# Kernel optimization log

Hardware: AMD Instinct MI355X
Metric: run time of the kernel (lower is better)

## Reference

```python
import jax, jax.numpy as jnp
import numpy as np

N_NODES = 50000
N_EDGES = 800000
N_GRAPHS = 64
IN_CH = 128
HID_CH = 128
OUT_CH = 2


def setup_inputs() -> dict:
    key = jax.random.key(0)
    k = jax.random.split(key, 7)
    x = jax.random.normal(k[0], (N_NODES, IN_CH), dtype=jnp.float32)
    edge_index = jax.random.randint(k[1], (2, N_EDGES), 0, N_NODES, dtype=jnp.int64)
    batch = jnp.sort(jax.random.randint(k[2], (N_NODES,), 0, N_GRAPHS, dtype=jnp.int64))
    W1 = jax.random.normal(k[3], (IN_CH, HID_CH), dtype=jnp.float32) * 0.05
    b1 = jnp.zeros((HID_CH,), dtype=jnp.float32)
    W2 = jax.random.normal(k[4], (HID_CH, OUT_CH), dtype=jnp.float32) * 0.05
    b2 = jnp.zeros((OUT_CH,), dtype=jnp.float32)
    return {"x": x, "edge_index": edge_index, "batch": batch,
            "W1": W1, "b1": b1, "W2": W2, "b2": b2}


def gcn_conv(x, edge_index, W, b):
    """PyG GCNConv: add self-loops, symmetric D^{-1/2}(A+I)D^{-1/2} aggregation of XW, plus bias."""
    n = x.shape[0]
    loop = jnp.arange(n, dtype=edge_index.dtype)
    src = jnp.concatenate([edge_index[0], loop])  # [E+N]
    dst = jnp.concatenate([edge_index[1], loop])
    ones = jnp.ones_like(dst, dtype=x.dtype)
    deg = jax.ops.segment_sum(ones, dst, num_segments=n)      # in-degree incl. self-loop (>=1)
    d_inv_sqrt = jax.lax.rsqrt(deg)
    norm = d_inv_sqrt[src] * d_inv_sqrt[dst]                  # [E+N]
    h = x @ W                                                 # [N, out]
    msg = h[src] * norm[:, None]                              # gather + scale
    out = jax.ops.segment_sum(msg, dst, num_segments=n)       # scatter-add
    return out + b


def global_mean_pool(x, batch, num_graphs):
    sums = jax.ops.segment_sum(x, batch, num_segments=num_graphs)
    cnt = jax.ops.segment_sum(jnp.ones((x.shape[0],), dtype=x.dtype), batch, num_segments=num_graphs)
    return sums / jnp.maximum(cnt, 1.0)[:, None]


def reference(x, edge_index, batch, W1, b1, W2, b2):
    h = jax.nn.relu(gcn_conv(x, edge_index, W1, b1))
    h = gcn_conv(h, edge_index, W2, b2)
    out = global_mean_pool(h, batch, N_GRAPHS)  # [G, out_channels]
    # dropout in eval mode == identity
    return out
```

## Files before the change

kernel.cpp:

```cpp
#include <hip/hip_runtime.h>


#define NGRAPH 64
#define CH 128
#define BSUB 384
#define NCOPY 8
#define BCAPT (BSUB * NCOPY)

typedef float f32x4 __attribute__((ext_vector_type(4)));
typedef _Float16 f16x8 __attribute__((ext_vector_type(8)));
typedef _Float16 f16x4 __attribute__((ext_vector_type(4)));
typedef _Float16 f16x2 __attribute__((ext_vector_type(2)));

__global__ void k_init(int* __restrict__ bcur8, int* __restrict__ row_start,
                       float* __restrict__ gsum, int* __restrict__ gcnt,
                       int NB, int N, int E) {
    int i = blockIdx.x * blockDim.x + threadIdx.x;
    if (i < NB * NCOPY) bcur8[i] = 0;
    if (i == 0) row_start[N] = E;
    if (i < 2 * NGRAPH) gsum[i] = 0.f;
    if (i < NGRAPH) gcnt[i] = 0;
}

__global__ __launch_bounds__(256) void k_bin(const int* __restrict__ src,
                                             const int* __restrict__ dst,
                                             int* __restrict__ bcur8,
                                             unsigned int* __restrict__ tmp,
                                             int E, int EPB) {
    __shared__ int hist[512];
    __shared__ int gbase[512];
    __shared__ int cur[512];
    int t = threadIdx.x;
    int e0 = blockIdx.x * EPB;
    int e1 = min(E, e0 + EPB);
    for (int i = t; i < 512; i += 256) { hist[i] = 0; cur[i] = 0; }
    __syncthreads();
    for (int e = e0 + t; e < e1; e += 256)
        atomicAdd(&hist[dst[e] >> 7], 1);
    __syncthreads();
    int copy = blockIdx.x & (NCOPY - 1);
    for (int b = t; b < 512; b += 256) {
        int hc = hist[b];
        if (hc) gbase[b] = atomicAdd(&bcur8[b * NCOPY + copy], hc);
    }
    __syncthreads();
    for (int e = e0 + t; e < e1; e += 256) {
        int d = dst[e];
        int b = d >> 7;
        int li = atomicAdd(&cur[b], 1);
        int pos = gbase[b] + li;
        if (pos < BSUB)
            tmp[(size_t)b * BCAPT + copy * BSUB + pos] =
                ((unsigned)(d & 127) << 25) | (unsigned)src[e];
    }
}

__global__ __launch_bounds__(256) void k_hist(const unsigned int* __restrict__ tmp,
                                              const int* __restrict__ bcur8,
                                              int* __restrict__ deg,
                                              float* __restrict__ dinv, int N) {
    __shared__ int hist[128];
    int b = blockIdx.x, t = threadIdx.x;
    if (t < 128) hist[t] = 0;
    __syncthreads();
    const unsigned int* tb = tmp + (size_t)b * BCAPT;
    for (int c = 0; c < NCOPY; c++) {
        int cnt = min(bcur8[b * NCOPY + c], BSUB);
        const unsigned int* tp = tb + c * BSUB;
        for (int e = t; e < cnt; e += 256) atomicAdd(&hist[tp[e] >> 25], 1);
    }
    __syncthreads();
    int n = b * 128 + t;
    if (t < 128 && n < N) {
        int d = hist[t] + 1;
        deg[n] = d;
        dinv[n] = rsqrtf((float)d);
    }
}

__global__ void k_scan_a(const int* __restrict__ deg, int* __restrict__ row_start,
                         int* __restrict__ bsum, int N) {
    __shared__ int tmp[256];
    int t = threadIdx.x;
    int i = blockIdx.x * 256 + t;
    int v = (i < N) ? (deg[i] - 1) : 0;
    int val = v;
    tmp[t] = val;
    __syncthreads();
    for (int off = 1; off < 256; off <<= 1) {
        int add = (t >= off) ? tmp[t - off] : 0;
        __syncthreads();
        val += add;
        tmp[t] = val;
        __syncthreads();
    }
    if (i < N) row_start[i] = val - v;
    if (t == 255) bsum[blockIdx.x] = val;
}

__global__ void k_scan_b(const int* __restrict__ bsum, int* __restrict__ boff, int nb) {
    __shared__ int tmp[256];
    int t = threadIdx.x;
    int v = (t < nb) ? bsum[t] : 0;
    int val = v;
    tmp[t] = val;
    __syncthreads();
    for (int off = 1; off < 256; off <<= 1) {
        int add = (t >= off) ? tmp[t - off] : 0;
        __syncthreads();
        val += add;
        tmp[t] = val;
        __syncthreads();
    }
    if (t < nb) boff[t] = val - v;
}

__global__ void k_scan_c(int* __restrict__ row_start, const int* __restrict__ boff, int N) {
    int i = blockIdx.x * blockDim.x + threadIdx.x;
    if (i < N) row_start[i] += boff[blockIdx.x];
}

__global__ __launch_bounds__(256) void k_place(const unsigned int* __restrict__ tmp,
                                               const int* __restrict__ bcur8,
                                               const int* __restrict__ row_start,
                                               int* __restrict__ csr, int N) {
    __shared__ int lcur[128];
    int b = blockIdx.x, t = threadIdx.x;
    int nb0 = b * 128;
    int base = row_start[nb0];
    if (t < 128) {
        int n = nb0 + t;
        lcur[t] = ((n < N) ? row_start[n] : 0) - base;
    }
    __syncthreads();
    const unsigned int* tb = tmp + (size_t)b * BCAPT;
    for (int c = 0; c < NCOPY; c++) {
        int cnt = min(bcur8[b * NCOPY + c], BSUB);
        const unsigned int* tp = tb + c * BSUB;
        for (int e = t; e < cnt; e += 256) {
            unsigned p = tp[e];
            int pos = atomicAdd(&lcur[p >> 25], 1);
            csr[base + pos] = (int)(p & 0x01FFFFFFu);
        }
    }
}

__global__ __launch_bounds__(256) void k_gemm1(const float* __restrict__ X,
                                               const float* __restrict__ W1,
                                               const float* __restrict__ dinv,
                                               _Float16* __restrict__ H, int N) {
    __shared__ _Float16 Xs[64 * 136];
    __shared__ _Float16 Ws[128 * 136];
    int t = threadIdx.x;
    int row0 = blockIdx.x * 64;
    const float4* Xv = (const float4*)X;
    const float4* Wv = (const float4*)W1;

    #pragma unroll
    for (int i = 0; i < 8; i++) {
        int gi = t + i * 256;
        int r = gi >> 5, c4 = gi & 31;
        int gr = row0 + r;
        float4 v = (gr < N) ? Xv[(size_t)gr * 32 + c4] : make_float4(0.f, 0.f, 0.f, 0.f);
        f16x4 hv = {(_Float16)v.x, (_Float16)v.y, (_Float16)v.z, (_Float16)v.w};
        *(f16x4*)&Xs[r * 136 + 4 * c4] = hv;
    }
    #pragma unroll
    for (int i = 0; i < 4; i++) {
        int b = t + i * 256;
        int kb = b >> 5, cb = b & 31;
        float4 r0 = Wv[(4 * kb + 0) * 32 + cb];
        float4 r1 = Wv[(4 * kb + 1) * 32 + cb];
        float4 r2 = Wv[(4 * kb + 2) * 32 + cb];
        float4 r3 = Wv[(4 * kb + 3) * 32 + cb];
        f16x4 c0v = {(_Float16)r0.x, (_Float16)r1.x, (_Float16)r2.x, (_Float16)r3.x};
        f16x4 c1v = {(_Float16)r0.y, (_Float16)r1.y, (_Float16)r2.y, (_Float16)r3.y};
        f16x4 c2v = {(_Float16)r0.z, (_Float16)r1.z, (_Float16)r2.z, (_Float16)r3.z};
        f16x4 c3v = {(_Float16)r0.w, (_Float16)r1.w, (_Float16)r2.w, (_Float16)r3.w};
        *(f16x4*)&Ws[(4 * cb + 0) * 136 + 4 * kb] = c0v;
        *(f16x4*)&Ws[(4 * cb + 1) * 136 + 4 * kb] = c1v;
        *(f16x4*)&Ws[(4 * cb + 2) * 136 + 4 * kb] = c2v;
        *(f16x4*)&Ws[(4 * cb + 3) * 136 + 4 * kb] = c3v;
    }
    __syncthreads();

    int w = t >> 6, l = t & 63;
    int r0w = w * 16;
    int lr = l & 15, lk = (l >> 4) * 8;
    f32x4 acc[8] = {};
    #pragma unroll
    for (int k0 = 0; k0 < 128; k0 += 32) {
        f16x8 a = *(const f16x8*)&Xs[(r0w + lr) * 136 + k0 + lk];
        #pragma unroll
        for (int c = 0; c < 8; c++) {
            f16x8 bf = *(const f16x8*)&Ws[(c * 16 + lr) * 136 + k0 + lk];
            acc[c] = __builtin_amdgcn_mfma_f32_16x16x32_f16(a, bf, acc[c], 0, 0, 0);
        }
    }
    float dv[4];
    #pragma unroll
    for (int q = 0; q < 4; q++) {
        int gr = row0 + r0w + (l >> 4) * 4 + q;
        dv[q] = (gr < N) ? dinv[gr] : 0.f;
    }
    __syncthreads();
    #pragma unroll
    for (int c = 0; c < 8; c++)
        #pragma unroll
        for (int q = 0; q < 4; q++)
            Xs[(r0w + (l >> 4) * 4 + q) * 136 + c * 16 + lr] = (_Float16)(acc[c][q] * dv[q]);
    __syncthreads();
    f16x2* Hv = (f16x2*)H;
    #pragma unroll
    for (int i = 0; i < 16; i++) {
        int gi = t + i * 256;
        int r = gi >> 6, cp = gi & 63;
        int gr = row0 + r;
        if (gr < N) Hv[(size_t)gr * 64 + cp] = *(f16x2*)&Xs[r * 136 + 2 * cp];
    }
}

__global__ __launch_bounds__(256) void k_layer1(const _Float16* __restrict__ h,
                                                const int* __restrict__ csr,
                                                const int* __restrict__ row_start,
                                                const float* __restrict__ dinv,
                                                const float* __restrict__ b1,
                                                const float* __restrict__ W2,
                                                float* __restrict__ h2, int N) {
    int n = (blockIdx.x * 256 + threadIdx.x) >> 6;
    int l = threadIdx.x & 63;
    if (n >= N) return;
    const f16x2* hv = (const f16x2*)h;
    float dn = dinv[n];
    f16x2 self = hv[(size_t)n * 64 + l];
    float acc0 = (float)self.x, acc1 = (float)self.y;
    int base = row_start[n];
    int cnt = row_start[n + 1] - base;
    for (int c0 = 0; c0 < cnt; c0 += 64) {
        int m = cnt - c0; if (m > 64) m = 64;
        int idx = (c0 + l < cnt) ? csr[base + c0 + l] : 0;
        int j = 0;
        int jm = m & ~7;
        for (; j < jm; j += 8) {
            int s0 = __shfl(idx, j + 0), s1 = __shfl(idx, j + 1);
            int s2 = __shfl(idx, j + 2), s3 = __shfl(idx, j + 3);
            int s4 = __shfl(idx, j + 4), s5 = __shfl(idx, j + 5);
            int s6 = __shfl(idx, j + 6), s7 = __shfl(idx, j + 7);
            f16x2 v0 = hv[(size_t)s0 * 64 + l];
            f16x2 v1 = hv[(size_t)s1 * 64 + l];
            f16x2 v2 = hv[(size_t)s2 * 64 + l];
            f16x2 v3 = hv[(size_t)s3 * 64 + l];
            f16x2 v4 = hv[(size_t)s4 * 64 + l];
            f16x2 v5 = hv[(size_t)s5 * 64 + l];
            f16x2 v6 = hv[(size_t)s6 * 64 + l];
            f16x2 v7 = hv[(size_t)s7 * 64 + l];
            acc0 += (float)v0.x; acc1 += (float)v0.y;
            acc0 += (float)v1.x; acc1 += (float)v1.y;
            acc0 += (float)v2.x; acc1 += (float)v2.y;
            acc0 += (float)v3.x; acc1 += (float)v3.y;
            acc0 += (float)v4.x; acc1 += (float)v4.y;
            acc0 += (float)v5.x; acc1 += (float)v5.y;
            acc0 += (float)v6.x; acc1 += (float)v6.y;
            acc0 += (float)v7.x; acc1 += (float)v7.y;
        }
        for (; j < m; ++j) {
            int s = __shfl(idx, j);
            f16x2 v = hv[(size_t)s * 64 + l];
            acc0 += (float)v.x; acc1 += (float)v.y;
        }
    }
    float2 bb = ((const float2*)b1)[l];
    float v0 = fmaxf(fmaf(dn, acc0, bb.x), 0.f);
    float v1 = fmaxf(fmaf(dn, acc1, bb.y), 0.f);
    float4 w2 = ((const float4*)W2)[l];
    float p0 = fmaf(v0, w2.x, v1 * w2.z);
    float p1 = fmaf(v0, w2.y, v1 * w2.w);
    #pragma unroll
    for (int off = 32; off; off >>= 1) {
        p0 += __shfl_xor(p0, off);
        p1 += __shfl_xor(p1, off);
    }
    if (l == 0) ((float2*)h2)[n] = make_float2(p0 * dn, p1 * dn);
}

__global__ __launch_bounds__(256) void k_layer2_pool(const float* __restrict__ h2,
                                                     const int* __restrict__ csr,
                                                     const int* __restrict__ row_start,
                                                     const float* __restrict__ dinv,
                                                     const int* __restrict__ batch,
                                                     float* __restrict__ gsum,
                                                     int* __restrict__ gcnt, int N) {
    __shared__ float ssum[2 * NGRAPH];
    __shared__ int scnt[NGRAPH];
    int t = threadIdx.x;
    if (t < 2 * NGRAPH) ssum[t] = 0.f;
    if (t < NGRAPH) scnt[t] = 0;
    __syncthreads();
    int n = blockIdx.x * blockDim.x + t;
    if (n < N) {
        const float2* h2v = (const float2*)h2;
        float dn = dinv[n];
        float2 a = h2v[n];
        int base = row_start[n], end = row_start[n + 1];
        for (int e = base; e < end; e++) {
            float2 v = h2v[csr[e]];
            a.x += v.x;
            a.y += v.y;
        }
        a.x *= dn;
        a.y *= dn;
        int g = batch[n];
        atomicAdd(&ssum[g * 2 + 0], a.x);
        atomicAdd(&ssum[g * 2 + 1], a.y);
        atomicAdd(&scnt[g], 1);
    }
    __syncthreads();
    if (t < 2 * NGRAPH) atomicAdd(&gsum[t], ssum[t]);
    if (t < NGRAPH) atomicAdd(&gcnt[t], scnt[t]);
}

__global__ void k_final(const float* __restrict__ gsum, const int* __restrict__ gcnt,
                        const float* __restrict__ b2, float* __restrict__ out) {
    int t = threadIdx.x;
    if (t < 2 * NGRAPH) {
        int g = t >> 1, c = t & 1;
        float cnt = fmaxf((float)gcnt[g], 1.f);
        out[t] = gsum[t] / cnt + b2[c];
    }
}

extern "C" void kernel_launch(void* const* d_in, const int* in_sizes, int n_in,
                              void* d_out, int out_size, void* d_ws, size_t ws_size,
                              hipStream_t stream) {
    const float* x     = (const float*)d_in[0];
    const int*   ei    = (const int*)d_in[1];
    const int*   batch = (const int*)d_in[2];
    const float* W1    = (const float*)d_in[3];
    const float* b1    = (const float*)d_in[4];
    const float* W2    = (const float*)d_in[5];
    const float* b2    = (const float*)d_in[6];
    float* out = (float*)d_out;

    int N = in_sizes[0] / CH;
    int E = in_sizes[1] / 2;
    int NB = (N + 127) / 128;
    const int* esrc = ei;
    const int* edst = ei + E;

    char* w = (char*)d_ws;
    auto alloc = [&](size_t bytes) -> void* {
        void* p = (void*)w;
        w += (bytes + 255) & ~(size_t)255;
        return p;
    };
    _Float16* h      = (_Float16*)alloc((size_t)N * CH * sizeof(_Float16));
    int* deg         = (int*)  alloc((size_t)N * sizeof(int));
    float* dinv      = (float*)alloc((size_t)N * sizeof(float));
    int* row_start   = (int*)  alloc((size_t)(N + 1) * sizeof(int));
    int* csr         = (int*)  alloc((size_t)E * sizeof(int));
    float* h2        = (float*)alloc((size_t)N * 2 * sizeof(float));
    int* bcur8       = (int*)  alloc((size_t)NB * NCOPY * sizeof(int));
    int* bsum        = (int*)  alloc(256 * sizeof(int));
    int* boff        = (int*)  alloc(256 * sizeof(int));
    float* gsum      = (float*)alloc(128 * sizeof(float));
    int* gcnt        = (int*)  alloc(64 * sizeof(int));
    unsigned int* tmp = (unsigned int*)h;

    int nbN = (N + 255) / 256;
    int NCHUNK = 256;
    int EPB = (E + NCHUNK - 1) / NCHUNK;

    k_init  <<<nbN, 256, 0, stream>>>(bcur8, row_start, gsum, gcnt, NB, N, E);
    k_bin   <<<NCHUNK, 256, 0, stream>>>(esrc, edst, bcur8, tmp, E, EPB);
    k_hist  <<<NB,  256, 0, stream>>>(tmp, bcur8, deg, dinv, N);
    k_scan_a<<<nbN, 256, 0, stream>>>(deg, row_start, bsum, N);
    k_scan_b<<<1,   256, 0, stream>>>(bsum, boff, nbN);
    k_scan_c<<<nbN, 256, 0, stream>>>(row_start, boff, N);
    k_place <<<NB,  256, 0, stream>>>(tmp, bcur8, row_start, csr, N);
    k_gemm1 <<<(N + 63) / 64, 256, 0, stream>>>(x, W1, dinv, h, N);
    k_layer1<<<(N * 64 + 255) / 256, 256, 0, stream>>>(h, csr, row_start, dinv, b1, W2, h2, N);
    k_layer2_pool<<<nbN, 256, 0, stream>>>(h2, csr, row_start, dinv, batch, gsum, gcnt, N);
    k_final <<<1, 128, 0, stream>>>(gsum, gcnt, b2, out);
}
```

Baseline: 185.5 us.

## Fuse degree histogram, scan and CSR placement into one build kernel

Replaces the separate histogram, three-pass scan and placement kernels with a single-block bucket-total scan followed by one build kernel per bucket. That kernel computes degrees, a local scan, row starts, dinv and CSR placement together. W1 is also converted to transposed fp16 once in the init kernel, so each GEMM block copies it instead of reconverting it. This cuts kernel launches and global round-trips for deg and row_start, at the cost of a serial 512-thread scan kernel.

Result: faster. 174.9 us (-5.7%).

```diff
diff --git a/kernel.cpp b/kernel.cpp
--- a/kernel.cpp
+++ b/kernel.cpp
@@ -14,12 +14,17 @@
 
 __global__ void k_init(int* __restrict__ bcur8, int* __restrict__ row_start,
                        float* __restrict__ gsum, int* __restrict__ gcnt,
+                       const float* __restrict__ W1, _Float16* __restrict__ w1t,
                        int NB, int N, int E) {
     int i = blockIdx.x * blockDim.x + threadIdx.x;
     if (i < NB * NCOPY) bcur8[i] = 0;
     if (i == 0) row_start[N] = E;
     if (i < 2 * NGRAPH) gsum[i] = 0.f;
     if (i < NGRAPH) gcnt[i] = 0;
+    if (i < CH * CH) {
+        int k = i >> 7, c = i & 127;
+        w1t[c * CH + k] = (_Float16)W1[i];
+    }
 }
 
 __global__ __launch_bounds__(256) void k_bin(const int* __restrict__ src,
@@ -55,11 +60,35 @@
     }
 }
 
-__global__ __launch_bounds__(256) void k_hist(const unsigned int* __restrict__ tmp,
-                                              const int* __restrict__ bcur8,
-                                              int* __restrict__ deg,
-                                              float* __restrict__ dinv, int N) {
+__global__ __launch_bounds__(512) void k_bsum(const int* __restrict__ bcur8,
+                                              int* __restrict__ bbase, int NB) {
+    __shared__ int tmp[512];
+    int t = threadIdx.x;
+    int v = 0;
+    if (t < NB)
+        for (int c = 0; c < NCOPY; c++) v += min(bcur8[t * NCOPY + c], BSUB);
+    int val = v;
+    tmp[t] = val;
+    __syncthreads();
+    for (int off = 1; off < 512; off <<= 1) {
+        int add = (t >= off) ? tmp[t - off] : 0;
+        __syncthreads();
+        val += add;
+        tmp[t] = val;
+        __syncthreads();
+    }
+    if (t < NB) bbase[t] = val - v;
+}
+
+__global__ __launch_bounds__(256) void k_build(const unsigned int* __restrict__ tmp,
+                                               const int* __restrict__ bcur8,
+                                               const int* __restrict__ bbase,
+                                               int* __restrict__ row_start,
+                                               float* __restrict__ dinv,
+                                               int* __restrict__ csr, int N) {
     __shared__ int hist[128];
+    __shared__ int scan[128];
+    __shared__ int lcur[128];
     int b = blockIdx.x, t = threadIdx.x;
     if (t < 128) hist[t] = 0;
     __syncthreads();
@@ -70,70 +99,26 @@
         for (int e = t; e < cnt; e += 256) atomicAdd(&hist[tp[e] >> 25], 1);
     }
     __syncthreads();
-    int n = b * 128 + t;
-    if (t < 128 && n < N) {
-        int d = hist[t] + 1;
-        deg[n] = d;
-        dinv[n] = rsqrtf((float)d);
-    }
-}
-
-__global__ void k_scan_a(const int* __restrict__ deg, int* __restrict__ row_start,
-                         int* __restrict__ bsum, int N) {
-    __shared__ int tmp[256];
-    int t = threadIdx.x;
-    int i = blockIdx.x * 256 + t;
-    int v = (i < N) ? (deg[i] - 1) : 0;
-    int val = v;
-    tmp[t] = val;
-    __syncthreads();
-    for (int off = 1; off < 256; off <<= 1) {
-        int add = (t >= off) ? tmp[t - off] : 0;
+    int val = 0, v = 0;
+    if (t < 128) { v = hist[t]; val = v; scan[t] = val; }
+    __syncthreads();
+    for (int off = 1; off < 128; off <<= 1) {
+        int add = (t >= off && t < 128) ? scan[t - off] : 0;
         __syncthreads();
-        val += add;
-        tmp[t] = val;
+        if (t < 128) { val += add; scan[t] = val; }
         __syncthreads();
     }
-    if (i < N) row_start[i] = val - v;
-    if (t == 255) bsum[blockIdx.x] = val;
-}
-
-__global__ void k_scan_b(const int* __restrict__ bsum, int* __restrict__ boff, int nb) {
-    __shared__ int tmp[256];
-    int t = threadIdx.x;
-    int v = (t < nb) ? bsum[t] : 0;
-    int val = v;
-    tmp[t] = val;
-    __syncthreads();
-    for (int off = 1; off < 256; off <<= 1) {
-        int add = (t >= off) ? tmp[t - off] : 0;
-        __syncthreads();
-        val += add;
-        tmp[t] = val;
-        __syncthreads();
-    }
-    if (t < nb) boff[t] = val - v;
-}
-
-__global__ void k_scan_c(int* __restrict__ row_start, const int* __restrict__ boff, int N) {
-    int i = blockIdx.x * blockDim.x + threadIdx.x;
-    if (i < N) row_start[i] += boff[blockIdx.x];
-}
-
-__global__ __launch_bounds__(256) void k_place(const unsigned int* __restrict__ tmp,
-                                               const int* __restrict__ bcur8,
-                                               const int* __restrict__ row_start,
-                                               int* __restrict__ csr, int N) {
-    __shared__ int lcur[128];
-    int b = blockIdx.x, t = threadIdx.x;
-    int nb0 = b * 128;
-    int base = row_start[nb0];
+    int base = bbase[b];
     if (t < 128) {
-        int n = nb0 + t;
-        lcur[t] = ((n < N) ? row_start[n] : 0) - base;
-    }
-    __syncthreads();
-    const unsigned int* tb = tmp + (size_t)b * BCAPT;
+        int excl = val - v;
+        lcur[t] = excl;
+        int n = b * 128 + t;
+        if (n < N) {
+            row_start[n] = base + excl;
+            dinv[n] = rsqrtf((float)(v + 1));
+        }
+    }
+    __syncthreads();
     for (int c = 0; c < NCOPY; c++) {
         int cnt = min(bcur8[b * NCOPY + c], BSUB);
         const unsigned int* tp = tb + c * BSUB;
@@ -146,7 +131,7 @@
 }
 
 __global__ __launch_bounds__(256) void k_gemm1(const float* __restrict__ X,
-                                               const float* __restrict__ W1,
+                                               const _Float16* __restrict__ w1t,
                                                const float* __restrict__ dinv,
                                                _Float16* __restrict__ H, int N) {
     __shared__ _Float16 Xs[64 * 136];
@@ -154,7 +139,6 @@
     int t = threadIdx.x;
     int row0 = blockIdx.x * 64;
     const float4* Xv = (const float4*)X;
-    const float4* Wv = (const float4*)W1;
 
     #pragma unroll
     for (int i = 0; i < 8; i++) {
@@ -166,21 +150,11 @@
         *(f16x4*)&Xs[r * 136 + 4 * c4] = hv;
     }
     #pragma unroll
-    for (int i = 0; i < 4; i++) {
-        int b = t + i * 256;
-        int kb = b >> 5, cb = b & 31;
-        float4 r0 = Wv[(4 * kb + 0) * 32 + cb];
-        float4 r1 = Wv[(4 * kb + 1) * 32 + cb];
-        float4 r2 = Wv[(4 * kb + 2) * 32 + cb];
-        float4 r3 = Wv[(4 * kb + 3) * 32 + cb];
-        f16x4 c0v = {(_Float16)r0.x, (_Float16)r1.x, (_Float16)r2.x, (_Float16)r3.x};
-        f16x4 c1v = {(_Float16)r0.y, (_Float16)r1.y, (_Float16)r2.y, (_Float16)r3.y};
-        f16x4 c2v = {(_Float16)r0.z, (_Float16)r1.z, (_Float16)r2.z, (_Float16)r3.z};
-        f16x4 c3v = {(_Float16)r0.w, (_Float16)r1.w, (_Float16)r2.w, (_Float16)r3.w};
-        *(f16x4*)&Ws[(4 * cb + 0) * 136 + 4 * kb] = c0v;
-        *(f16x4*)&Ws[(4 * cb + 1) * 136 + 4 * kb] = c1v;
-        *(f16x4*)&Ws[(4 * cb + 2) * 136 + 4 * kb] = c2v;
-        *(f16x4*)&Ws[(4 * cb + 3) * 136 + 4 * kb] = c3v;
+    for (int i = 0; i < 8; i++) {
+        int gi = t + i * 256;
+        int r = gi >> 4, cc = gi & 15;
+        f16x8 vv = *(const f16x8*)&w1t[r * CH + cc * 8];
+        *(f16x8*)&Ws[r * 136 + cc * 8] = vv;
     }
     __syncthreads();
 
@@ -354,14 +328,13 @@
         return p;
     };
     _Float16* h      = (_Float16*)alloc((size_t)N * CH * sizeof(_Float16));
-    int* deg         = (int*)  alloc((size_t)N * sizeof(int));
     float* dinv      = (float*)alloc((size_t)N * sizeof(float));
     int* row_start   = (int*)  alloc((size_t)(N + 1) * sizeof(int));
     int* csr         = (int*)  alloc((size_t)E * sizeof(int));
     float* h2        = (float*)alloc((size_t)N * 2 * sizeof(float));
     int* bcur8       = (int*)  alloc((size_t)NB * NCOPY * sizeof(int));
-    int* bsum        = (int*)  alloc(256 * sizeof(int));
-    int* boff        = (int*)  alloc(256 * sizeof(int));
+    int* bbase       = (int*)  alloc((size_t)NB * sizeof(int));
+    _Float16* w1t    = (_Float16*)alloc((size_t)CH * CH * sizeof(_Float16));
     float* gsum      = (float*)alloc(128 * sizeof(float));
     int* gcnt        = (int*)  alloc(64 * sizeof(int));
     unsigned int* tmp = (unsigned int*)h;
@@ -370,14 +343,11 @@
     int NCHUNK = 256;
     int EPB = (E + NCHUNK - 1) / NCHUNK;
 
-    k_init  <<<nbN, 256, 0, stream>>>(bcur8, row_start, gsum, gcnt, NB, N, E);
+    k_init  <<<64, 256, 0, stream>>>(bcur8, row_start, gsum, gcnt, W1, w1t, NB, N, E);
     k_bin   <<<NCHUNK, 256, 0, stream>>>(esrc, edst, bcur8, tmp, E, EPB);
-    k_hist  <<<NB,  256, 0, stream>>>(tmp, bcur8, deg, dinv, N);
-    k_scan_a<<<nbN, 256, 0, stream>>>(deg, row_start, bsum, N);
-    k_scan_b<<<1,   256, 0, stream>>>(bsum, boff, nbN);
-    k_scan_c<<<nbN, 256, 0, stream>>>(row_start, boff, N);
-    k_place <<<NB,  256, 0, stream>>>(tmp, bcur8, row_start, csr, N);
-    k_gemm1 <<<(N + 63) / 64, 256, 0, stream>>>(x, W1, dinv, h, N);
+    k_bsum  <<<1, 512, 0, stream>>>(bcur8, bbase, NB);
+    k_build <<<NB, 256, 0, stream>>>(tmp, bcur8, bbase, row_start, dinv, csr, N);
+    k_gemm1 <<<(N + 63) / 64, 256, 0, stream>>>(x, w1t, dinv, h, N);
     k_layer1<<<(N * 64 + 255) / 256, 256, 0, stream>>>(h, csr, row_start, dinv, b1, W2, h2, N);
     k_layer2_pool<<<nbN, 256, 0, stream>>>(h2, csr, row_start, dinv, batch, gsum, gcnt, N);
     k_final <<<1, 128, 0, stream>>>(gsum, gcnt, b2, out);
```
